# Performance work log

Measured on AMD Instinct MI355X. Metric: run time of the kernel, lower is better.

## Reference

```python
import jax, jax.numpy as jnp
import numpy as np

GROUPS = 32
EPS = 1e-5


def setup_inputs() -> dict:
    key = jax.random.key(0)
    ks = jax.random.split(key, 6)
    B, H, W, C = 2, 64, 64, 512
    wscale = 0.02  # keep logits in a sane range for softmax
    return {
        "x": jax.random.normal(ks[0], (B, H, W, C), dtype=jnp.float32),
        "gamma": jnp.ones((C,), jnp.float32),
        "beta": jnp.zeros((C,), jnp.float32),
        "wq": jax.random.normal(ks[1], (C, C), dtype=jnp.float32) * wscale,
        "bq": jnp.zeros((C,), jnp.float32),
        "wk": jax.random.normal(ks[2], (C, C), dtype=jnp.float32) * wscale,
        "bk": jnp.zeros((C,), jnp.float32),
        "wv": jax.random.normal(ks[3], (C, C), dtype=jnp.float32) * wscale,
        "bv": jnp.zeros((C,), jnp.float32),
        "wp": jax.random.normal(ks[4], (C, C), dtype=jnp.float32) * wscale,
        "bp": jnp.zeros((C,), jnp.float32),
    }


def _group_norm(x, gamma, beta):
    B, H, W, C = x.shape
    xg = x.reshape(B, H, W, GROUPS, C // GROUPS)
    mean = xg.mean(axis=(1, 2, 4), keepdims=True)
    var = xg.var(axis=(1, 2, 4), keepdims=True)
    xn = ((xg - mean) * jax.lax.rsqrt(var + EPS)).reshape(B, H, W, C)
    return xn * gamma + beta


def reference(x, gamma, beta, wq, bq, wk, bk, wv, bv, wp, bp):
    B, H, W, C = x.shape
    xn = _group_norm(x, gamma, beta)
    # 1x1 convs == per-pixel linear layers
    q = (xn @ wq + bq).reshape(B, H * W, C)
    k = (xn @ wk + bk).reshape(B, H * W, C)
    v = (xn @ wv + bv).reshape(B, H * W, C)
    scale = C ** (-0.5)
    attn = jax.nn.softmax(jnp.einsum("bqc,bkc->bqk", q, k) * scale, axis=-1)
    out = jnp.einsum("bqk,bkc->bqc", attn, v).reshape(B, H, W, C)
    return (out @ wp + bp) + x
```

## Files before the change

kernel.cpp:

```cpp
#include <hip/hip_runtime.h>


typedef __bf16 bf16_t;
typedef __bf16 bf16x8 __attribute__((ext_vector_type(8)));
typedef __bf16 bf16x4 __attribute__((ext_vector_type(4)));
typedef float  f32x4  __attribute__((ext_vector_type(4)));

__device__ __forceinline__ bf16x8 ld8(const bf16_t* p) {
    return *reinterpret_cast<const bf16x8*>(p);
}
__device__ __forceinline__ f32x4 mfma16(bf16x8 a, bf16x8 b, f32x4 c) {
    return __builtin_amdgcn_mfma_f32_16x16x32_bf16(a, b, c, 0, 0, 0);
}
__device__ __forceinline__ void gload16(const bf16_t* gp, bf16_t* lp) {
    __builtin_amdgcn_global_load_lds(
        (const __attribute__((address_space(1))) void*)gp,
        (__attribute__((address_space(3))) void*)lp, 16, 0, 0);
}

#define NPIX 8192
#define C512 512
#define SEQ  4096
#define QSCALE 0.044194173824159216f

__global__ __launch_bounds__(256) void gn_sum_k(const float* __restrict__ x,
                                                float* __restrict__ accum) {
    int bg    = blockIdx.x >> 3;
    int slice = blockIdx.x & 7;
    int b = bg >> 5, g = bg & 31;
    const float* xp = x + (size_t)b * SEQ * C512 + g * 16;
    float s = 0.f, s2 = 0.f;
    #pragma unroll
    for (int pp = 0; pp < 2; pp++) {
        int p = slice * 512 + pp * 256 + threadIdx.x;
        const float4* q = reinterpret_cast<const float4*>(xp + (size_t)p * C512);
        #pragma unroll
        for (int i = 0; i < 4; i++) {
            float4 v = q[i];
            s  += v.x + v.y + v.z + v.w;
            s2 += v.x*v.x + v.y*v.y + v.z*v.z + v.w*v.w;
        }
    }
    #pragma unroll
    for (int off = 32; off >= 1; off >>= 1) {
        s  += __shfl_down(s, off);
        s2 += __shfl_down(s2, off);
    }
    __shared__ float rs[4], rs2[4];
    int wave = threadIdx.x >> 6;
    if ((threadIdx.x & 63) == 0) { rs[wave] = s; rs2[wave] = s2; }
    __syncthreads();
    if (threadIdx.x == 0) {
        float S = rs[0] + rs[1] + rs[2] + rs[3];
        float S2 = rs2[0] + rs2[1] + rs2[2] + rs2[3];
        atomicAdd(&accum[bg * 2],     S);
        atomicAdd(&accum[bg * 2 + 1], S2);
    }
}

__global__ __launch_bounds__(256) void wt_conv_k(const float* wq, const float* wk,
                                                 const float* wv, const float* wp,
                                                 bf16_t* wqkvT, bf16_t* wpT) {
    int y = blockIdx.y;
    const float* w = (y == 0) ? wq : (y == 1) ? wk : (y == 2) ? wv : wp;
    float scale = (y == 0) ? QSCALE : 1.0f;
    int tid = blockIdx.x * 256 + threadIdx.x;
    int n = tid >> 9, k = tid & 511;
    bf16_t val = (bf16_t)(w[(size_t)k * C512 + n] * scale);
    if (y < 3) wqkvT[((size_t)y * C512 + n) * C512 + k] = val;
    else       wpT[(size_t)n * C512 + k] = val;
}

__global__ __launch_bounds__(256) void bias_merge_k(const float* bq, const float* bk,
                                                    const float* bv, float* bqkv) {
    int i = blockIdx.x * 256 + threadIdx.x;
    float v = (i < 512) ? bq[i] * QSCALE : (i < 1024) ? bk[i - 512] : bv[i - 1024];
    bqkv[i] = v;
}

__global__ __launch_bounds__(256) void xn_k(const float* __restrict__ x,
                                            const float* __restrict__ accum,
                                            const float* __restrict__ gamma,
                                            const float* __restrict__ beta,
                                            bf16_t* __restrict__ xn) {
    size_t idx = ((size_t)blockIdx.x * 256 + threadIdx.x) * 4;
    int c = (int)(idx & 511);
    size_t pix = idx >> 9;
    int b = (int)(pix >> 12);
    int g = c >> 4;
    float sum = accum[(b * 32 + g) * 2];
    float ssq = accum[(b * 32 + g) * 2 + 1];
    float mean = sum * (1.f / 65536.f);
    float var  = ssq * (1.f / 65536.f) - mean * mean;
    float rstd = rsqrtf(var + 1e-5f);
    float4 v  = *reinterpret_cast<const float4*>(x + idx);
    float4 gm = *reinterpret_cast<const float4*>(gamma + c);
    float4 bt = *reinterpret_cast<const float4*>(beta + c);
    bf16x4 o;
    o[0] = (bf16_t)((v.x - mean) * rstd * gm.x + bt.x);
    o[1] = (bf16_t)((v.y - mean) * rstd * gm.y + bt.y);
    o[2] = (bf16_t)((v.z - mean) * rstd * gm.z + bt.z);
    o[3] = (bf16_t)((v.w - mean) * rstd * gm.w + bt.w);
    *reinterpret_cast<bf16x4*>(xn + idx) = o;
}

template <int MODE>
__global__ __launch_bounds__(256, 2) void gemm128_k(
        const bf16_t* __restrict__ Aall, const bf16_t* __restrict__ Ball,
        const float* __restrict__ bias, const float* __restrict__ resid,
        void* __restrict__ out0, void* __restrict__ out1,
        void* __restrict__ out2, void* __restrict__ out3,
        float* __restrict__ lsum) {
    constexpr int TM  = (MODE == 3) ? 64 : 128;
    constexpr int ASZ = TM * 32;
    constexpr int ACH = TM / 16;
    constexpr int CPW = (ACH + 8) / 4;
    constexpr int MI  = TM / 32;
    __shared__ bf16_t smem[2 * ASZ + 8192];

    int lane = threadIdx.x & 63;
    int w    = threadIdx.x >> 6;
    int wr   = w >> 1, wc = w & 1;
    int lrow = lane & 15, quad = lane >> 4;

    const bf16_t* A = Aall;
    const bf16_t* B = Ball;
    size_t lda = 512, ldb = 512;
    int ksteps = 16;

    int bm = blockIdx.x * TM, bn = blockIdx.y * 128;

    auto stage = [&](int buf, int ks) {
        size_t k0 = (size_t)ks * 32;
        #pragma unroll
        for (int ii = 0; ii < CPW; ii++) {
            int c = w * CPW + ii;
            if (c < ACH) {
                const bf16_t* gpA = A + (size_t)(bm + c * 16 + lrow) * lda + k0 + quad * 8;
                gload16(gpA, &smem[buf * ASZ + c * 512]);
            } else {
                int cb = c - ACH;
                const bf16_t* gpB = B + (size_t)(bn + cb * 16 + lrow) * ldb + k0 + quad * 8;
                gload16(gpB, &smem[2 * ASZ + buf * 4096 + cb * 512]);
            }
        }
    };

    f32x4 acc[MI][4] = {};

    stage(0, 0);

    for (int ks = 0; ks < ksteps; ks++) {
        int cur = ks & 1;
        __syncthreads();
        if (ks + 1 < ksteps) stage(1 - cur, ks + 1);

        const bf16_t* al = &smem[cur * ASZ + (wr * MI) * 512];
        const bf16_t* bl = &smem[2 * ASZ + cur * 4096 + (wc * 4) * 512];
        bf16x8 af[MI], bf[4];
        #pragma unroll
        for (int m = 0; m < MI; m++) af[m] = ld8(al + m * 512 + lane * 8);
        #pragma unroll
        for (int n = 0; n < 4; n++) bf[n] = ld8(bl + n * 512 + lane * 8);
        #pragma unroll
        for (int m = 0; m < MI; m++)
            #pragma unroll
            for (int n = 0; n < 4; n++)
                acc[m][n] = mfma16(af[m], bf[n], acc[m][n]);
    }

    #pragma unroll
    for (int m = 0; m < MI; m++) {
        int rowb = bm + wr * (TM / 2) + m * 16 + quad * 4;
        #pragma unroll
        for (int n = 0; n < 4; n++) {
            int col = bn + wc * 64 + n * 16 + lrow;
            #pragma unroll
            for (int i = 0; i < 4; i++) {
                int row = rowb + i;
                float v = acc[m][n][i];
                if (MODE == 0) {
                    int seg = col >> 9, c = col & 511;
                    bf16_t val = (bf16_t)(v + bias[col]);
                    if (seg == 0) {
                        ((bf16_t*)out0)[(size_t)row * C512 + c] = val;
                    } else if (seg == 1) {
                        ((bf16_t*)out1)[(size_t)row * C512 + c] = val;
                    } else {
                        int b = row >> 12, s = row & 4095;
                        ((bf16_t*)out2)[((size_t)(b * C512 + c)) * SEQ + s] = val;
                    }
                } else {
                    size_t idx = (size_t)row * C512 + col;
                    ((float*)out0)[idx] = v + bias[col] + resid[idx];
                }
            }
        }
    }
}

__global__ __launch_bounds__(512, 1) void fattn_k(
        const bf16_t* __restrict__ Q, const bf16_t* __restrict__ K,
        const bf16_t* __restrict__ VT, bf16_t* __restrict__ Op0,
        bf16_t* __restrict__ Op1, float* __restrict__ lsum) {
    __shared__ bf16_t Kl[2][32 * 512];
    __shared__ bf16_t Vl[2][32 * 512];
    __shared__ bf16_t Pl[2][64 * 32];

    int bid = blockIdx.x;
    int xcd = bid & 7, loc = bid >> 3;
    int b   = (xcd >> 1) & 1;
    int kv  = xcd & 1;
    int q0  = ((xcd >> 2) * 32 + loc) * 64;
    int key0 = kv * 2048;

    const bf16_t* Qb = Q  + (size_t)b * SEQ * C512;
    const bf16_t* Kb = K  + (size_t)b * SEQ * C512;
    const bf16_t* Vb = VT + (size_t)b * C512 * SEQ;
    bf16_t* Op = kv ? Op1 : Op0;

    int lane = threadIdx.x & 63;
    int w    = threadIdx.x >> 6;
    int lrow = lane & 15, quad = lane >> 4;

    #pragma unroll
    for (int ii = 0; ii < 4; ii++) {
        int cc = w * 4 + ii;
        int ks = cc >> 1, ktc = cc & 1;
        const bf16_t* gp = Kb + (size_t)(key0 + ktc * 16 + lrow) * C512 + ks * 32 + quad * 8;
        gload16(gp, &Kl[0][cc * 512]);
    }
    __syncthreads();

    if (w < 4) {
        int qh = w >> 1, kt = w & 1;
        bf16x8 qf[2][16];
        const bf16_t* qp = Qb + (size_t)(q0 + qh * 32 + lrow) * C512 + quad * 8;
        #pragma unroll
        for (int m = 0; m < 2; m++)
            #pragma unroll
            for (int ks = 0; ks < 16; ks++)
                qf[m][ks] = ld8(qp + (size_t)m * 16 * C512 + ks * 32);
        float rs[2][4] = {};

        for (int i = 0; i <= 64; ++i) {
            int cur = i & 1;
            if (i < 64) {
                if (i < 63) {
                    #pragma unroll
                    for (int ii = 0; ii < 8; ii++) {
                        int cc = w * 8 + ii;
                        int ks = cc >> 1, ktc = cc & 1;
                        const bf16_t* gp = Kb +
                            (size_t)(key0 + (i + 1) * 32 + ktc * 16 + lrow) * C512 +
                            ks * 32 + quad * 8;
                        gload16(gp, &Kl[cur ^ 1][cc * 512]);
                    }
                }
                f32x4 sacc0 = {}, sacc1 = {};
                #pragma unroll
                for (int ks = 0; ks < 16; ks++) {
                    bf16x8 kf = ld8(&Kl[cur][(ks * 2 + kt) * 512 + lane * 8]);
                    sacc0 = mfma16(qf[0][ks], kf, sacc0);
                    sacc1 = mfma16(qf[1][ks], kf, sacc1);
                }
                #pragma unroll
                for (int i4 = 0; i4 < 4; i4++) {
                    float p0 = __expf(fminf(sacc0[i4], 20.0f));
                    float p1 = __expf(fminf(sacc1[i4], 20.0f));
                    rs[0][i4] += p0;
                    rs[1][i4] += p1;
                    int obase = (quad * 4 + i4) * 8 +
                                (kt * 2 + (lrow >> 3)) * 128 + (lrow & 7);
                    Pl[cur][(qh * 2 + 0) * 512 + obase] = (bf16_t)p0;
                    Pl[cur][(qh * 2 + 1) * 512 + obase] = (bf16_t)p1;
                }
            }
            __syncthreads();
        }
        #pragma unroll
        for (int m = 0; m < 2; m++) {
            #pragma unroll
            for (int i4 = 0; i4 < 4; i4++) {
                float r = rs[m][i4];
                r += __shfl_xor(r, 1);
                r += __shfl_xor(r, 2);
                r += __shfl_xor(r, 4);
                r += __shfl_xor(r, 8);
                if (lrow == 0)
                    atomicAdd(&lsum[(size_t)b * SEQ + q0 + qh * 32 + m * 16 +
                                    quad * 4 + i4], r);
            }
        }
    } else {
        int u = w - 4;
        f32x4 acc[4][8] = {};
        for (int i = 0; i <= 64; ++i) {
            int cur = i & 1;
            if (i < 64) {
                #pragma unroll
                for (int ii = 0; ii < 8; ii++) {
                    int ct = u * 8 + ii;
                    const bf16_t* gp = Vb + (size_t)(ct * 16 + lrow) * SEQ +
                                       key0 + i * 32 + quad * 8;
                    gload16(gp, &Vl[cur][ct * 512]);
                }
            }
            if (i >= 1) {
                int pb = cur ^ 1;
                bf16x8 pa[4];
                #pragma unroll
                for (int mm = 0; mm < 4; mm++)
                    pa[mm] = ld8(&Pl[pb][mm * 512 + lane * 8]);
                #pragma unroll
                for (int n = 0; n < 8; n++) {
                    bf16x8 vf = ld8(&Vl[pb][(u * 8 + n) * 512 + lane * 8]);
                    #pragma unroll
                    for (int mm = 0; mm < 4; mm++)
                        acc[mm][n] = mfma16(pa[mm], vf, acc[mm][n]);
                }
            }
            __syncthreads();
        }
        #pragma unroll
        for (int mm = 0; mm < 4; mm++) {
            int row = q0 + mm * 16 + quad * 4;
            #pragma unroll
            for (int n = 0; n < 8; n++) {
                int col = u * 128 + n * 16 + lrow;
                #pragma unroll
                for (int i4 = 0; i4 < 4; i4++)
                    Op[((size_t)b * SEQ + row + i4) * C512 + col] =
                        (bf16_t)acc[mm][n][i4];
            }
        }
    }
}

__global__ __launch_bounds__(256) void attn_combine2_k(
        const bf16_t* __restrict__ Op0, const bf16_t* __restrict__ Op1,
        const float* __restrict__ lsum, bf16_t* __restrict__ O) {
    int idx = blockIdx.x * 256 + threadIdx.x;
    int row = idx >> 6;
    int c8  = (idx & 63) << 3;
    float inv = 1.0f / lsum[row];
    size_t base = (size_t)row * C512 + c8;
    bf16x8 o0 = ld8(Op0 + base), o1 = ld8(Op1 + base);
    bf16x8 o;
    #pragma unroll
    for (int j = 0; j < 8; j++)
        o[j] = (bf16_t)(((float)o0[j] + (float)o1[j]) * inv);
    *reinterpret_cast<bf16x8*>(O + base) = o;
}

extern "C" void kernel_launch(void* const* d_in, const int* in_sizes, int n_in,
                              void* d_out, int out_size, void* d_ws, size_t ws_size,
                              hipStream_t stream) {
    const float* x     = (const float*)d_in[0];
    const float* gamma = (const float*)d_in[1];
    const float* beta  = (const float*)d_in[2];
    const float* wq = (const float*)d_in[3];  const float* bq = (const float*)d_in[4];
    const float* wk = (const float*)d_in[5];  const float* bk = (const float*)d_in[6];
    const float* wv = (const float*)d_in[7];  const float* bv = (const float*)d_in[8];
    const float* wp = (const float*)d_in[9];  const float* bp = (const float*)d_in[10];
    float* out = (float*)d_out;

    char* ws = (char*)d_ws;
    size_t off = 0;
    float*  bqkv   = (float*)(ws + off);   off += 1536 * sizeof(float);
    float*  lsum   = (float*)(ws + off);   off += (size_t)NPIX * sizeof(float);
    float*  accum  = (float*)(ws + off);   off += 128 * sizeof(float);
    bf16_t* xn     = (bf16_t*)(ws + off);  off += (size_t)NPIX * C512 * 2;
    bf16_t* wqkvT  = (bf16_t*)(ws + off);  off += (size_t)3 * C512 * C512 * 2;
    bf16_t* wpT    = (bf16_t*)(ws + off);  off += (size_t)C512 * C512 * 2;
    bf16_t* Qb     = (bf16_t*)(ws + off);  off += (size_t)NPIX * C512 * 2;
    bf16_t* Kb     = (bf16_t*)(ws + off);  off += (size_t)NPIX * C512 * 2;
    bf16_t* VTb    = (bf16_t*)(ws + off);  off += (size_t)NPIX * C512 * 2;
    bf16_t* Op0    = (bf16_t*)(ws + off);  off += (size_t)NPIX * C512 * 2;
    bf16_t* Op1    = (bf16_t*)(ws + off);  off += (size_t)NPIX * C512 * 2;
    bf16_t* Ob  = xn;

    hipMemsetAsync(lsum, 0, (size_t)(NPIX + 128) * sizeof(float), stream);

    gn_sum_k<<<512, 256, 0, stream>>>(x, accum);
    wt_conv_k<<<dim3(1024, 4), 256, 0, stream>>>(wq, wk, wv, wp, wqkvT, wpT);
    bias_merge_k<<<6, 256, 0, stream>>>(bq, bk, bv, bqkv);
    xn_k<<<4096, 256, 0, stream>>>(x, accum, gamma, beta, xn);

    gemm128_k<0><<<dim3(64, 12, 1), 256, 0, stream>>>(
        xn, wqkvT, bqkv, nullptr, Qb, Kb, VTb, nullptr, nullptr);

    fattn_k<<<256, 512, 0, stream>>>(Qb, Kb, VTb, Op0, Op1, lsum);

    attn_combine2_k<<<2048, 256, 0, stream>>>(Op0, Op1, lsum, Ob);

    gemm128_k<3><<<dim3(128, 4, 1), 256, 0, stream>>>(
        Ob, wpT, bp, x, out, nullptr, nullptr, nullptr, nullptr);
}
```

Baseline: 320.0 us.

## Load K and V fragments directly from global memory instead of LDS staging

Removes the double-buffered LDS staging of K and V tiles in the split-warp flash-attention kernel. Each warp now reads its MFMA operand fragments straight from global memory (relying on L2/cache) and splits the QK accumulation into two independent chains. The __syncthreads calls become a bare s_barrier after lgkmcnt wait, and s_setprio is raised around the MFMA loops. This frees LDS and drops the async copy and sync overhead, but global-load latency is now exposed inside the compute loop without prefetch, and K/V traffic is no longer shared across warps.

```diff
diff --git a/kernel.cpp b/kernel.cpp
--- a/kernel.cpp
+++ b/kernel.cpp
@@ -203,8 +203,6 @@
         const bf16_t* __restrict__ Q, const bf16_t* __restrict__ K,
         const bf16_t* __restrict__ VT, bf16_t* __restrict__ Op0,
         bf16_t* __restrict__ Op1, float* __restrict__ lsum) {
-    __shared__ bf16_t Kl[2][32 * 512];
-    __shared__ bf16_t Vl[2][32 * 512];
     __shared__ bf16_t Pl[2][64 * 32];
 
     int bid = blockIdx.x;
@@ -223,15 +221,6 @@
     int w    = threadIdx.x >> 6;
     int lrow = lane & 15, quad = lane >> 4;
 
-    #pragma unroll
-    for (int ii = 0; ii < 4; ii++) {
-        int cc = w * 4 + ii;
-        int ks = cc >> 1, ktc = cc & 1;
-        const bf16_t* gp = Kb + (size_t)(key0 + ktc * 16 + lrow) * C512 + ks * 32 + quad * 8;
-        gload16(gp, &Kl[0][cc * 512]);
-    }
-    __syncthreads();
-
     if (w < 4) {
         int qh = w >> 1, kt = w & 1;
         bf16x8 qf[2][16];
@@ -242,28 +231,25 @@
             for (int ks = 0; ks < 16; ks++)
                 qf[m][ks] = ld8(qp + (size_t)m * 16 * C512 + ks * 32);
         float rs[2][4] = {};
+        const bf16_t* kbase = Kb + (size_t)(key0 + kt * 16 + lrow) * C512 + quad * 8;
 
         for (int i = 0; i <= 64; ++i) {
             int cur = i & 1;
             if (i < 64) {
-                if (i < 63) {
-                    #pragma unroll
-                    for (int ii = 0; ii < 8; ii++) {
-                        int cc = w * 8 + ii;
-                        int ks = cc >> 1, ktc = cc & 1;
-                        const bf16_t* gp = Kb +
-                            (size_t)(key0 + (i + 1) * 32 + ktc * 16 + lrow) * C512 +
-                            ks * 32 + quad * 8;
-                        gload16(gp, &Kl[cur ^ 1][cc * 512]);
-                    }
+                const bf16_t* kp = kbase + (size_t)i * 32 * C512;
+                f32x4 s0a = {}, s0b = {}, s1a = {}, s1b = {};
+                __builtin_amdgcn_s_setprio(1);
+                #pragma unroll
+                for (int ks = 0; ks < 8; ks++) {
+                    bf16x8 kfa = ld8(kp + (2 * ks) * 32);
+                    bf16x8 kfb = ld8(kp + (2 * ks + 1) * 32);
+                    s0a = mfma16(qf[0][2 * ks],     kfa, s0a);
+                    s1a = mfma16(qf[1][2 * ks],     kfa, s1a);
+                    s0b = mfma16(qf[0][2 * ks + 1], kfb, s0b);
+                    s1b = mfma16(qf[1][2 * ks + 1], kfb, s1b);
                 }
-                f32x4 sacc0 = {}, sacc1 = {};
-                #pragma unroll
-                for (int ks = 0; ks < 16; ks++) {
-                    bf16x8 kf = ld8(&Kl[cur][(ks * 2 + kt) * 512 + lane * 8]);
-                    sacc0 = mfma16(qf[0][ks], kf, sacc0);
-                    sacc1 = mfma16(qf[1][ks], kf, sacc1);
-                }
+                __builtin_amdgcn_s_setprio(0);
+                f32x4 sacc0 = s0a + s0b, sacc1 = s1a + s1b;
                 #pragma unroll
                 for (int i4 = 0; i4 < 4; i4++) {
                     float p0 = __expf(fminf(sacc0[i4], 20.0f));
@@ -276,7 +262,9 @@
                     Pl[cur][(qh * 2 + 1) * 512 + obase] = (bf16_t)p1;
                 }
             }
-            __syncthreads();
+            asm volatile("s_waitcnt lgkmcnt(0)" ::: "memory");
+            __builtin_amdgcn_s_barrier();
+            __builtin_amdgcn_sched_barrier(0);
         }
         #pragma unroll
         for (int m = 0; m < 2; m++) {
@@ -297,30 +285,27 @@
         f32x4 acc[4][8] = {};
         for (int i = 0; i <= 64; ++i) {
             int cur = i & 1;
-            if (i < 64) {
-                #pragma unroll
-                for (int ii = 0; ii < 8; ii++) {
-                    int ct = u * 8 + ii;
-                    const bf16_t* gp = Vb + (size_t)(ct * 16 + lrow) * SEQ +
-                                       key0 + i * 32 + quad * 8;
-                    gload16(gp, &Vl[cur][ct * 512]);
-                }
-            }
             if (i >= 1) {
                 int pb = cur ^ 1;
+                const bf16_t* vp = Vb + (size_t)(u * 128 + lrow) * SEQ +
+                                   key0 + (i - 1) * 32 + quad * 8;
                 bf16x8 pa[4];
                 #pragma unroll
                 for (int mm = 0; mm < 4; mm++)
                     pa[mm] = ld8(&Pl[pb][mm * 512 + lane * 8]);
+                __builtin_amdgcn_s_setprio(1);
                 #pragma unroll
                 for (int n = 0; n < 8; n++) {
-                    bf16x8 vf = ld8(&Vl[pb][(u * 8 + n) * 512 + lane * 8]);
+                    bf16x8 vf = ld8(vp + (size_t)(n * 16) * SEQ);
                     #pragma unroll
                     for (int mm = 0; mm < 4; mm++)
                         acc[mm][n] = mfma16(pa[mm], vf, acc[mm][n]);
                 }
-            }
-            __syncthreads();
+                __builtin_amdgcn_s_setprio(0);
+            }
+            asm volatile("s_waitcnt lgkmcnt(0)" ::: "memory");
+            __builtin_amdgcn_s_barrier();
+            __builtin_amdgcn_sched_barrier(0);
         }
         #pragma unroll
         for (int mm = 0; mm < 4; mm++) {
```

Result: slower. 419.3 us (+31.0%).
